# Optimization experiments

Measured on AMD Instinct MI355X. Metric: run time of the kernel, lower is better.

The kernel has to match this reference:

```python
import jax, jax.numpy as jnp
import numpy as np

HEAD, STACK = 8, 2
EPS = 1e-5


def _ln2d(x):
    # F.layer_norm(x, x.size()[1:]): normalize over (seq, feature) jointly, no affine
    m = jnp.mean(x, axis=(1, 2), keepdims=True)
    v = jnp.var(x, axis=(1, 2), keepdims=True)
    return (x - m) / jnp.sqrt(v + EPS)


def setup_inputs() -> dict:
    key = jax.random.key(0)
    ks = jax.random.split(key, 8)
    B, S, V, E, D, C = 64, 1024, 8000, 200, 200, 31
    g = lambda k, shape, sc: (jax.random.normal(k, shape, jnp.float32) * sc)
    return dict(
        x=jax.random.randint(ks[0], (B, S), 0, V),
        embed=g(ks[1], (V, E), 0.02),
        pos=g(ks[2], (S, E), 0.02),
        Wp=g(ks[3], (E, D), 0.05), bp=jnp.zeros((D,), jnp.float32),
        Wm=g(ks[4], (D * HEAD, D), 0.05), bm=jnp.zeros((D,), jnp.float32),
        W1=g(ks[5], (D, D), 0.05), b1=jnp.zeros((D,), jnp.float32),
        W2=g(ks[6], (D, D), 0.05), b2=jnp.zeros((D,), jnp.float32),
        Wd=g(ks[7], (D, C), 0.05), bd=jnp.zeros((C,), jnp.float32),
    )


def reference(x, embed, pos, Wp, bp, Wm, bm, W1, b1, W2, b2, Wd, bd):
    h = embed[x] + pos                       # [B,S,200]
    scale = jnp.sqrt(jnp.asarray(Wp.shape[1], jnp.float32))
    for _ in range(STACK):                   # weights shared across stacks (aliased in torch)
        r = h
        p = h @ Wp + bp                      # q = k = v (same aliased Linear in torch)
        a = jax.nn.softmax(jnp.einsum('bsd,btd->bst', p, p) / scale, axis=-1)
        c = jnp.einsum('bst,btd->bsd', a, p)  # [B,S,200]
        cat = jnp.tile(c, (1, 1, HEAD))       # all heads identical -> concat = tile
        h = _ln2d(cat @ Wm + bm + r)
        r = h
        ff = jax.nn.relu(h @ W1 + b1) @ W2 + b2
        h = _ln2d(ff + r)
    return h[:, -1, :] @ Wd + bd             # [B, class_num]; dropout = identity (eval)
```

## Files before the change

kernel.cpp:

```cpp
#include <hip/hip_runtime.h>
#include <cstddef>
#include <cstdint>
#include <cmath>

#define BDIM  64
#define SDIM  1024
#define DDIM  200
#define DPAD  224
#define PSTRIDE 232
#define CDIM  31
#define NSTACK 2
#define EPS   1e-5f
#define LN_N  204800.0f

typedef __attribute__((ext_vector_type(8))) short short8;
typedef __attribute__((ext_vector_type(4))) short short4_t;
typedef __attribute__((ext_vector_type(4))) float f32x4;

__device__ __forceinline__ short f2bf(float f) {
    union { float f; unsigned u; } v; v.f = f;
    unsigned r = v.u + 0x7FFFu + ((v.u >> 16) & 1u);
    return (short)(r >> 16);
}
__device__ __forceinline__ float bf2f(short s) {
    union { unsigned u; float f; } v; v.u = ((unsigned)(unsigned short)s) << 16;
    return v.f;
}
__device__ __forceinline__ unsigned cvtpk_bf16(float a, float b) {
    unsigned r;
    asm volatile("v_cvt_pk_bf16_f32 %0, %1, %2" : "=v"(r) : "v"(a), "v"(b));
    return r;
}
__device__ __forceinline__ void gload_lds16(const short* g, short* l) {
    __builtin_amdgcn_global_load_lds(
        (const __attribute__((address_space(1))) void*)g,
        (__attribute__((address_space(3))) void*)l, 16, 0, 0);
}

__global__ void prep_kernel(const float* __restrict__ Wp, const float* __restrict__ bp,
                            const float* __restrict__ Wm, const float* __restrict__ bm,
                            const float* __restrict__ W1, const float* __restrict__ b1,
                            const float* __restrict__ W2, const float* __restrict__ b2,
                            short* __restrict__ WtP, short* __restrict__ WtM,
                            short* __restrict__ Wt1, short* __restrict__ Wt2,
                            float* __restrict__ bpP, float* __restrict__ bmP,
                            float* __restrict__ b1P, float* __restrict__ b2P,
                            float* __restrict__ csP, float* __restrict__ cs1)
{
    int idx = blockIdx.x * 256 + threadIdx.x;
    if (idx >= DPAD * DPAD) return;
    int n = idx / DPAD, k = idx - n * DPAD;
    bool valid = (n < DDIM) && (k < DDIM);
    WtP[idx] = valid ? f2bf(Wp[(size_t)k * DDIM + n]) : 0;
    Wt1[idx] = valid ? f2bf(W1[(size_t)k * DDIM + n]) : 0;
    Wt2[idx] = valid ? f2bf(W2[(size_t)k * DDIM + n]) : 0;
    float s = 0.f;
    if (valid) {
        #pragma unroll
        for (int blk = 0; blk < 8; ++blk)
            s += Wm[(size_t)(blk * DDIM + k) * DDIM + n];
    }
    WtM[idx] = valid ? f2bf(s) : 0;
    if (idx < DPAD) {
        bpP[idx] = idx < DDIM ? bp[idx] : 0.f;
        bmP[idx] = idx < DDIM ? bm[idx] : 0.f;
        b1P[idx] = idx < DDIM ? b1[idx] : 0.f;
        b2P[idx] = idx < DDIM ? b2[idx] : 0.f;
        float sp = 0.f, s1 = 0.f;
        if (idx < DDIM) {
            for (int kk = 0; kk < DDIM; ++kk) {
                sp += bf2f(f2bf(Wp[(size_t)kk * DDIM + idx]));
                s1 += bf2f(f2bf(W1[(size_t)kk * DDIM + idx]));
            }
        }
        csP[idx] = sp;
        cs1[idx] = s1;
    }
}

__global__ void embed_kernel(const int* __restrict__ x, const float* __restrict__ embed,
                             const float* __restrict__ pos, short* __restrict__ h)
{
    const int row = blockIdx.x;
    const int n = threadIdx.x;
    if (n >= DPAD) return;
    const int s = row & (SDIM - 1);
    const int tok = x[row];
    float v = (n < DDIM) ? embed[(size_t)tok * DDIM + n] + pos[(size_t)s * DDIM + n] : 0.f;
    h[(size_t)row * DPAD + n] = (n < DDIM) ? f2bf(v) : (short)0;
}

#define WSLICE 7168
#define GBUFSZ 11264
__global__ __launch_bounds__(256, 2)
void gemm_bf(const short* __restrict__ act, const float* __restrict__ actParts,
             const short* __restrict__ Wt, const float* __restrict__ bias,
             const float* __restrict__ csW,
             const short* __restrict__ res, const float* __restrict__ resParts,
             short* __restrict__ out, float* __restrict__ parts,
             int doRelu, int outStride)
{
    __shared__ short SB[2][GBUFSZ];

    const int tid  = threadIdx.x;
    const int wave = tid >> 6, lane = tid & 63;
    const int lo   = lane & 15, hi = lane >> 4;
    const int mblk = blockIdx.x * 128;

    auto stage = [&](int ks, int buf) {
        for (int c = wave; c < 22; c += 4) {
            if (c < 14) {
                int row = c * 16 + (lane >> 2);
                int kc  = (lane & 3) ^ ((row >> 1) & 3);
                gload_lds16(Wt + (size_t)row * DPAD + ks * 32 + kc * 8,
                            &SB[buf][c * 512 + lane * 8]);
            } else {
                int ci  = c - 14;
                int row = ci * 16 + (lane >> 2);
                int kc  = (lane & 3) ^ ((row >> 1) & 3);
                gload_lds16(act + (size_t)(mblk + row) * DPAD + ks * 32 + kc * 8,
                            &SB[buf][WSLICE + ci * 512 + lane * 8]);
            }
        }
    };

    f32x4 acc[2][14];
    #pragma unroll
    for (int mt = 0; mt < 2; ++mt)
        #pragma unroll
        for (int nt = 0; nt < 14; ++nt) acc[mt][nt] = (f32x4){0.f, 0.f, 0.f, 0.f};

    stage(0, 0);
    __syncthreads();

    #pragma unroll
    for (int ks = 0; ks < 7; ++ks) {
        const int cur = ks & 1;
        if (ks < 6) stage(ks + 1, cur ^ 1);

        short8 af[2];
        #pragma unroll
        for (int mt = 0; mt < 2; ++mt) {
            int arow = wave * 32 + mt * 16 + lo;
            af[mt] = *(const short8*)&SB[cur][WSLICE + arow * 32
                                             + ((hi * 8) ^ (((arow >> 1) & 3) << 3))];
        }
        #pragma unroll
        for (int nt = 0; nt < 14; ++nt) {
            int brow = nt * 16 + lo;
            short8 bf_ = *(const short8*)&SB[cur][brow * 32
                                                 + ((hi * 8) ^ (((brow >> 1) & 3) << 3))];
            acc[0][nt] = __builtin_amdgcn_mfma_f32_16x16x32_bf16(af[0], bf_, acc[0][nt], 0, 0, 0);
            acc[1][nt] = __builtin_amdgcn_mfma_f32_16x16x32_bf16(af[1], bf_, acc[1][nt], 0, 0, 0);
        }
        __syncthreads();
    }

    const int bb = mblk >> 10;
    float inv_a = 1.f, corr = 0.f;
    if (actParts) {
        float mean = actParts[bb * 2] / LN_N;
        inv_a = rsqrtf(actParts[bb * 2 + 1] / LN_N - mean * mean + EPS);
        corr = mean * inv_a;
    }
    float mean_r = 0.f, inv_r = 1.f;
    if (resParts) {
        mean_r = resParts[bb * 2] / LN_N;
        inv_r = rsqrtf(resParts[bb * 2 + 1] / LN_N - mean_r * mean_r + EPS);
    }

    float s = 0.f, s2 = 0.f;
    #pragma unroll
    for (int mt = 0; mt < 2; ++mt) {
        #pragma unroll
        for (int nt = 0; nt < 14; ++nt) {
            const int n = nt * 16 + lo;
            const float bn = bias[n];
            const float cw = actParts ? csW[n] : 0.f;
            float v[4];
            #pragma unroll
            for (int r = 0; r < 4; ++r)
                v[r] = acc[mt][nt][r] * inv_a + bn - corr * cw;
            if (res) {
                #pragma unroll
                for (int r = 0; r < 4; ++r) {
                    int m = mblk + wave * 32 + mt * 16 + hi * 4 + r;
                    v[r] += (bf2f(res[(size_t)m * DPAD + n]) - mean_r) * inv_r;
                }
            }
            if (doRelu)
                #pragma unroll
                for (int r = 0; r < 4; ++r) v[r] = fmaxf(v[r], 0.f);
            if (n >= DDIM)
                #pragma unroll
                for (int r = 0; r < 4; ++r) v[r] = 0.f;
            if (parts)
                #pragma unroll
                for (int r = 0; r < 4; ++r) { s += v[r]; s2 = fmaf(v[r], v[r], s2); }
            #pragma unroll
            for (int r = 0; r < 4; ++r) {
                int m = mblk + wave * 32 + mt * 16 + hi * 4 + r;
                out[(size_t)m * outStride + n] = f2bf(v[r]);
            }
        }
    }

    if (parts) {
        __shared__ float rs[4], rq[4];
        #pragma unroll
        for (int off = 32; off; off >>= 1) {
            s  += __shfl_down(s, off);
            s2 += __shfl_down(s2, off);
        }
        if (lane == 0) { rs[wave] = s; rq[wave] = s2; }
        __syncthreads();
        if (tid == 0) {
            atomicAdd(&parts[bb * 2],     rs[0] + rs[1] + rs[2] + rs[3]);
            atomicAdd(&parts[bb * 2 + 1], rq[0] + rq[1] + rq[2] + rq[3]);
        }
    }
}

__global__ void vt_kernel(const short* __restrict__ p, short* __restrict__ pt)
{
    __shared__ short T[32][33];
    const int b  = blockIdx.z;
    const int s0 = blockIdx.x * 32;
    const int d0 = blockIdx.y * 32;
    const int t  = threadIdx.x;
    const int row = t >> 3, c4 = (t & 7) * 4;
    short4_t v = *(const short4_t*)(p + ((size_t)b * SDIM + s0 + row) * PSTRIDE + d0 + c4);
    #pragma unroll
    for (int j = 0; j < 4; ++j) T[row][c4 + j] = v[j];
    __syncthreads();
    short4_t o;
    #pragma unroll
    for (int j = 0; j < 4; ++j) o[j] = T[c4 + j][row];
    *(short4_t*)(pt + ((size_t)b * DPAD + d0 + row) * SDIM + s0 + c4) = o;
}

__global__ __launch_bounds__(256, 2)
void attn_kernel(const short* __restrict__ pbf, const short* __restrict__ pt,
                 short* __restrict__ c, float qscale)
{
    __shared__ short Kbuf[2][7680];
    __shared__ short Vbuf[2][6656];

    const int bid = blockIdx.x;
    const int wg  = (bid & 7) * 64 + (bid >> 3);
    const int b   = wg >> 3;
    const int q0  = (wg & 7) * 128;

    const int tid  = threadIdx.x;
    const int wave = tid >> 6;
    const int lane = tid & 63;
    const int lo   = lane & 15;
    const int hi   = lane >> 4;

    const short* pb  = pbf + (size_t)b * SDIM * PSTRIDE;
    const short* ptb = pt  + (size_t)b * DPAD * SDIM;

    auto stage = [&](int kt2, int bufIdx) {
        const short* ks = pb + (size_t)kt2 * 32 * PSTRIDE + lane * 8;
        #pragma unroll
        for (int i = 0; i < 15; ++i)
            gload_lds16(ks + i * 512, &Kbuf[bufIdx][i * 512]);
        #pragma unroll
        for (int i = 0; i < 13; ++i) {
            int e = i * 512 + lane * 8;
            int d = e >> 5;
            int cc = (e & 31) ^ (((d >> 1) & 3) << 3);
            gload_lds16(ptb + (size_t)d * SDIM + kt2 * 32 + cc, &Vbuf[bufIdx][i * 512]);
        }
    };

    short8 qf[2][7];
    #pragma unroll
    for (int qt = 0; qt < 2; ++qt)
        #pragma unroll
        for (int ks = 0; ks < 7; ++ks) {
            short8 q = *(const short8*)(pb + (size_t)(q0 + wave * 32 + qt * 16 + lo) * PSTRIDE
                                        + ks * 32 + hi * 8);
            short8 qs;
            #pragma unroll
            for (int j = 0; j < 8; ++j) qs[j] = f2bf(bf2f(q[j]) * qscale);
            qf[qt][ks] = qs;
        }

    f32x4 o[2][13];
    float m[2], ell[2];
    #pragma unroll
    for (int qt = 0; qt < 2; ++qt) {
        #pragma unroll
        for (int n = 0; n < 13; ++n) o[qt][n] = (f32x4){0.f, 0.f, 0.f, 0.f};
        m[qt] = -1e30f; ell[qt] = 0.f;
    }

    if (wave == 0) stage(0, 0);
    __syncthreads();

    for (int kt = 0; kt < 32; ++kt) {
        const int cur = kt & 1;
        if (kt < 31 && wave == ((kt + 1) & 3)) stage(kt + 1, cur ^ 1);

        f32x4 sacc[2][2];
        #pragma unroll
        for (int qt = 0; qt < 2; ++qt)
            #pragma unroll
            for (int t = 0; t < 2; ++t) sacc[qt][t] = (f32x4){0.f, 0.f, 0.f, 0.f};
        __builtin_amdgcn_s_setprio(1);
        #pragma unroll
        for (int t = 0; t < 2; ++t)
            #pragma unroll
            for (int ks = 0; ks < 7; ++ks) {
                short8 kf = *(const short8*)(&Kbuf[cur][(t * 16 + lo) * PSTRIDE + ks * 32 + hi * 8]);
                sacc[0][t] = __builtin_amdgcn_mfma_f32_16x16x32_bf16(kf, qf[0][ks], sacc[0][t], 0, 0, 0);
                sacc[1][t] = __builtin_amdgcn_mfma_f32_16x16x32_bf16(kf, qf[1][ks], sacc[1][t], 0, 0, 0);
            }
        __builtin_amdgcn_s_setprio(0);

        short8 pa[2];
        #pragma unroll
        for (int qt = 0; qt < 2; ++qt) {
            float mx = fmaxf(fmaxf(fmaxf(sacc[qt][0][0], sacc[qt][0][1]),
                                   fmaxf(sacc[qt][0][2], sacc[qt][0][3])),
                             fmaxf(fmaxf(sacc[qt][1][0], sacc[qt][1][1]),
                                   fmaxf(sacc[qt][1][2], sacc[qt][1][3])));
            mx = fmaxf(mx, __shfl_xor(mx, 16));
            mx = fmaxf(mx, __shfl_xor(mx, 32));
            if (__any(mx > m[qt] + 11.5f)) {
                float mn = fmaxf(m[qt], mx);
                float al = exp2f(m[qt] - mn);
                m[qt] = mn; ell[qt] *= al;
                float alr[4];
                #pragma unroll
                for (int r = 0; r < 4; ++r) alr[r] = __shfl(al, hi * 4 + r);
                #pragma unroll
                for (int n = 0; n < 13; ++n)
                    #pragma unroll
                    for (int r = 0; r < 4; ++r) o[qt][n][r] *= alr[r];
            }
            float p[2][4]; float rsum = 0.f;
            #pragma unroll
            for (int t = 0; t < 2; ++t)
                #pragma unroll
                for (int r = 0; r < 4; ++r) {
                    p[t][r] = exp2f(sacc[qt][t][r] - m[qt]);
                    rsum += p[t][r];
                }
            rsum += __shfl_xor(rsum, 16);
            rsum += __shfl_xor(rsum, 32);
            ell[qt] += rsum;
            unsigned pk01_0 = cvtpk_bf16(p[0][0], p[0][1]);
            unsigned pk23_0 = cvtpk_bf16(p[0][2], p[0][3]);
            unsigned pk01_1 = cvtpk_bf16(p[1][0], p[1][1]);
            unsigned pk23_1 = cvtpk_bf16(p[1][2], p[1][3]);
            const int srcA = lo + ((hi & 1) * 2) * 16;
            const int srcB = srcA + 16;
            int a0 = __shfl((int)pk01_0, srcA), a1 = __shfl((int)pk01_1, srcA);
            int b0 = __shfl((int)pk23_0, srcA), b1 = __shfl((int)pk23_1, srcA);
            int c0 = __shfl((int)pk01_0, srcB), c1 = __shfl((int)pk01_1, srcB);
            int d0 = __shfl((int)pk23_0, srcB), d1 = __shfl((int)pk23_1, srcB);
            const bool thi = (hi >> 1) != 0;
            union { short8 s; int u[4]; } pu;
            pu.u[0] = thi ? a1 : a0;
            pu.u[1] = thi ? b1 : b0;
            pu.u[2] = thi ? c1 : c0;
            pu.u[3] = thi ? d1 : d0;
            pa[qt] = pu.s;
        }

        __builtin_amdgcn_s_setprio(1);
        #pragma unroll
        for (int n = 0; n < 13; ++n) {
            int d = n * 16 + lo;
            int addr = d * 32 + ((hi * 8) ^ (((d >> 1) & 3) << 3));
            short8 vf = *(const short8*)(&Vbuf[cur][addr]);
            o[0][n] = __builtin_amdgcn_mfma_f32_16x16x32_bf16(pa[0], vf, o[0][n], 0, 0, 0);
            o[1][n] = __builtin_amdgcn_mfma_f32_16x16x32_bf16(pa[1], vf, o[1][n], 0, 0, 0);
        }
        __builtin_amdgcn_s_setprio(0);

        __syncthreads();
    }

    #pragma unroll
    for (int qt = 0; qt < 2; ++qt) {
        float inv_l = 1.f / ell[qt];
        float invr[4];
        #pragma unroll
        for (int r = 0; r < 4; ++r) invr[r] = __shfl(inv_l, hi * 4 + r);
        #pragma unroll
        for (int n = 0; n < 13; ++n) {
            int dcol = n * 16 + lo;
            #pragma unroll
            for (int r = 0; r < 4; ++r) {
                size_t row = (size_t)b * SDIM + q0 + wave * 32 + qt * 16 + hi * 4 + r;
                c[row * DPAD + dcol] = f2bf(o[qt][n][r] * invr[r]);
            }
        }
        #pragma unroll
        for (int r = 0; r < 4; ++r) {
            size_t row = (size_t)b * SDIM + q0 + wave * 32 + qt * 16 + hi * 4 + r;
            c[row * DPAD + 208 + lo] = 0;
        }
    }
}

__global__ void final_kernel(const short* __restrict__ y, const float* __restrict__ parts,
                             const float* __restrict__ Wd, const float* __restrict__ bd,
                             float* __restrict__ out)
{
    const int b = blockIdx.x;
    const float sum = parts[b * 2], sq = parts[b * 2 + 1];
    const float mean = sum / LN_N;
    const float inv  = rsqrtf(sq / LN_N - mean * mean + EPS);
    __shared__ float hrow[DDIM];
    const short* row = y + ((size_t)b * SDIM + SDIM - 1) * DPAD;
    for (int d = threadIdx.x; d < DDIM; d += blockDim.x)
        hrow[d] = (bf2f(row[d]) - mean) * inv;
    __syncthreads();
    if (threadIdx.x < CDIM) {
        float acc = bd[threadIdx.x];
        for (int d = 0; d < DDIM; ++d)
            acc = fmaf(hrow[d], Wd[(size_t)d * CDIM + threadIdx.x], acc);
        out[(size_t)b * CDIM + threadIdx.x] = acc;
    }
}

extern "C" void kernel_launch(void* const* d_in, const int* in_sizes, int n_in,
                              void* d_out, int out_size, void* d_ws, size_t ws_size,
                              hipStream_t stream)
{
    const int*   x     = (const int*)  d_in[0];
    const float* embed = (const float*)d_in[1];
    const float* pos   = (const float*)d_in[2];
    const float* Wp    = (const float*)d_in[3];
    const float* bp    = (const float*)d_in[4];
    const float* Wm    = (const float*)d_in[5];
    const float* bm    = (const float*)d_in[6];
    const float* W1    = (const float*)d_in[7];
    const float* b1    = (const float*)d_in[8];
    const float* W2    = (const float*)d_in[9];
    const float* b2    = (const float*)d_in[10];
    const float* Wd    = (const float*)d_in[11];
    const float* bd    = (const float*)d_in[12];
    float* out = (float*)d_out;

    const size_t HB = (size_t)BDIM * SDIM * DPAD;
    const size_t PB = (size_t)BDIM * SDIM * PSTRIDE;

    short* h_bf  = (short*)d_ws;
    short* p_bf  = h_bf  + HB;
    short* pt    = p_bf  + PB;
    short* cb_bf = pt    + HB;
    short* yA    = cb_bf + HB;
    short* yB    = yA    + HB;
    short* WtP   = yB + HB;
    short* WtM   = WtP + DPAD * DPAD;
    short* Wt1   = WtM + DPAD * DPAD;
    short* Wt2   = Wt1 + DPAD * DPAD;
    float* bpP   = (float*)(Wt2 + DPAD * DPAD);
    float* bmP   = bpP + DPAD;
    float* b1P   = bmP + DPAD;
    float* b2P   = b1P + DPAD;
    float* csP   = b2P + DPAD;
    float* cs1   = csP + DPAD;
    float* parts = cs1 + DPAD;
    const size_t need = (size_t)((char*)(parts + 4 * BDIM * 2) - (char*)d_ws);
    if (ws_size < need) return;

    float* pA1 = parts;
    float* pB1 = parts + BDIM * 2;
    float* pA2 = parts + 2 * BDIM * 2;
    float* pB2 = parts + 3 * BDIM * 2;

    prep_kernel<<<dim3((DPAD * DPAD + 255) / 256), dim3(256), 0, stream>>>(
        Wp, bp, Wm, bm, W1, b1, W2, b2, WtP, WtM, Wt1, Wt2, bpP, bmP, b1P, b2P, csP, cs1);
    embed_kernel<<<dim3(BDIM * SDIM), dim3(256), 0, stream>>>(x, embed, pos, h_bf);
    hipMemsetAsync(parts, 0, 4 * BDIM * 2 * sizeof(float), stream);

    const float qscale = 1.44269504f / sqrtf((float)DDIM);
    const dim3 tgrid(SDIM / 32, DPAD / 32, BDIM);

    gemm_bf<<<dim3(512), dim3(256), 0, stream>>>(h_bf, nullptr, WtP, bpP, nullptr,
                                                 nullptr, nullptr, p_bf, nullptr, 0, PSTRIDE);
    vt_kernel<<<tgrid, dim3(256), 0, stream>>>(p_bf, pt);
    attn_kernel<<<dim3(512), dim3(256), 0, stream>>>(p_bf, pt, cb_bf, qscale);
    gemm_bf<<<dim3(512), dim3(256), 0, stream>>>(cb_bf, nullptr, WtM, bmP, nullptr,
                                                 h_bf, nullptr, yA, pA1, 0, DPAD);
    gemm_bf<<<dim3(512), dim3(256), 0, stream>>>(yA, pA1, Wt1, b1P, cs1,
                                                 nullptr, nullptr, cb_bf, nullptr, 1, DPAD);
    gemm_bf<<<dim3(512), dim3(256), 0, stream>>>(cb_bf, nullptr, Wt2, b2P, nullptr,
                                                 yA, pA1, yB, pB1, 0, DPAD);
    gemm_bf<<<dim3(512), dim3(256), 0, stream>>>(yB, pB1, WtP, bpP, csP,
                                                 nullptr, nullptr, p_bf, nullptr, 0, PSTRIDE);
    vt_kernel<<<tgrid, dim3(256), 0, stream>>>(p_bf, pt);
    attn_kernel<<<dim3(512), dim3(256), 0, stream>>>(p_bf, pt, cb_bf, qscale);
    gemm_bf<<<dim3(512), dim3(256), 0, stream>>>(cb_bf, nullptr, WtM, bmP, nullptr,
                                                 yB, pB1, h_bf, pA2, 0, DPAD);
    gemm_bf<<<dim3(512), dim3(256), 0, stream>>>(h_bf, pA2, Wt1, b1P, cs1,
                                                 nullptr, nullptr, cb_bf, nullptr, 1, DPAD);
    gemm_bf<<<dim3(512), dim3(256), 0, stream>>>(cb_bf, nullptr, Wt2, b2P, nullptr,
                                                 h_bf, pA2, yA, pB2, 0, DPAD);
    final_kernel<<<dim3(BDIM), dim3(64), 0, stream>>>(yA, pB2, Wd, bd, out);
}
```

Baseline: 436.3 us.

## Software-pipeline attention QK/PV, stage GEMM epilogue via LDS, vectorize embed

The attention loop is restructured so the QK^T scores and softmax for tile kt+1 are computed while the PV MFMAs for tile kt run. K and V are staged separately, with K prefetched two tiles ahead, and the rescale of the output accumulator is applied after PV. The GEMM epilogue now writes accumulators to LDS as bf16 and then does row-contiguous vectorized loads and stores of bias, residual and output, replacing scattered 2-byte accesses. The embed kernel becomes a grid-stride loop with float4 loads. Round-tripping accumulators through bf16 before bias and normalization adds rounding error, and the pipelining raises register pressure.

```diff
diff --git a/kernel.cpp b/kernel.cpp
--- a/kernel.cpp
+++ b/kernel.cpp
@@ -81,17 +81,28 @@
 __global__ void embed_kernel(const int* __restrict__ x, const float* __restrict__ embed,
                              const float* __restrict__ pos, short* __restrict__ h)
 {
-    const int row = blockIdx.x;
-    const int n = threadIdx.x;
-    if (n >= DPAD) return;
-    const int s = row & (SDIM - 1);
-    const int tok = x[row];
-    float v = (n < DDIM) ? embed[(size_t)tok * DDIM + n] + pos[(size_t)s * DDIM + n] : 0.f;
-    h[(size_t)row * DPAD + n] = (n < DDIM) ? f2bf(v) : (short)0;
+    const int total = BDIM * SDIM * (DPAD / 4);
+    for (int i = blockIdx.x * 256 + threadIdx.x; i < total; i += gridDim.x * 256) {
+        const int row = i / (DPAD / 4);
+        const int n0  = (i - row * (DPAD / 4)) * 4;
+        short4_t o;
+        if (n0 >= DDIM) {
+            o[0] = o[1] = o[2] = o[3] = 0;
+        } else {
+            const int s = row & (SDIM - 1);
+            const int tok = x[row];
+            const float4 e  = *(const float4*)(embed + (size_t)tok * DDIM + n0);
+            const float4 p4 = *(const float4*)(pos + (size_t)s * DDIM + n0);
+            o[0] = f2bf(e.x + p4.x); o[1] = f2bf(e.y + p4.y);
+            o[2] = f2bf(e.z + p4.z); o[3] = f2bf(e.w + p4.w);
+        }
+        *(short4_t*)(h + (size_t)row * DPAD + n0) = o;
+    }
 }
 
 #define WSLICE 7168
 #define GBUFSZ 11264
+#define SSTRIDE 236
 __global__ __launch_bounds__(256, 2)
 void gemm_bf(const short* __restrict__ act, const float* __restrict__ actParts,
              const short* __restrict__ Wt, const float* __restrict__ bias,
@@ -100,7 +111,7 @@
              short* __restrict__ out, float* __restrict__ parts,
              int doRelu, int outStride)
 {
-    __shared__ short SB[2][GBUFSZ];
+    __shared__ short MEM[128 * SSTRIDE];
 
     const int tid  = threadIdx.x;
     const int wave = tid >> 6, lane = tid & 63;
@@ -108,18 +119,19 @@
     const int mblk = blockIdx.x * 128;
 
     auto stage = [&](int ks, int buf) {
+        short* base = buf ? (MEM + GBUFSZ) : MEM;
         for (int c = wave; c < 22; c += 4) {
             if (c < 14) {
                 int row = c * 16 + (lane >> 2);
                 int kc  = (lane & 3) ^ ((row >> 1) & 3);
                 gload_lds16(Wt + (size_t)row * DPAD + ks * 32 + kc * 8,
-                            &SB[buf][c * 512 + lane * 8]);
+                            base + c * 512 + lane * 8);
             } else {
                 int ci  = c - 14;
                 int row = ci * 16 + (lane >> 2);
                 int kc  = (lane & 3) ^ ((row >> 1) & 3);
                 gload_lds16(act + (size_t)(mblk + row) * DPAD + ks * 32 + kc * 8,
-                            &SB[buf][WSLICE + ci * 512 + lane * 8]);
+                            base + WSLICE + ci * 512 + lane * 8);
             }
         }
     };
@@ -137,24 +149,35 @@
     for (int ks = 0; ks < 7; ++ks) {
         const int cur = ks & 1;
         if (ks < 6) stage(ks + 1, cur ^ 1);
+        const short* B_ = cur ? (MEM + GBUFSZ) : MEM;
 
         short8 af[2];
         #pragma unroll
         for (int mt = 0; mt < 2; ++mt) {
             int arow = wave * 32 + mt * 16 + lo;
-            af[mt] = *(const short8*)&SB[cur][WSLICE + arow * 32
-                                             + ((hi * 8) ^ (((arow >> 1) & 3) << 3))];
+            af[mt] = *(const short8*)&B_[WSLICE + arow * 32
+                                         + ((hi * 8) ^ (((arow >> 1) & 3) << 3))];
         }
         #pragma unroll
         for (int nt = 0; nt < 14; ++nt) {
             int brow = nt * 16 + lo;
-            short8 bf_ = *(const short8*)&SB[cur][brow * 32
-                                                 + ((hi * 8) ^ (((brow >> 1) & 3) << 3))];
+            short8 bf_ = *(const short8*)&B_[brow * 32
+                                             + ((hi * 8) ^ (((brow >> 1) & 3) << 3))];
             acc[0][nt] = __builtin_amdgcn_mfma_f32_16x16x32_bf16(af[0], bf_, acc[0][nt], 0, 0, 0);
             acc[1][nt] = __builtin_amdgcn_mfma_f32_16x16x32_bf16(af[1], bf_, acc[1][nt], 0, 0, 0);
         }
         __syncthreads();
     }
+
+    #pragma unroll
+    for (int mt = 0; mt < 2; ++mt)
+        #pragma unroll
+        for (int nt = 0; nt < 14; ++nt)
+            #pragma unroll
+            for (int r = 0; r < 4; ++r)
+                MEM[(wave * 32 + mt * 16 + hi * 4 + r) * SSTRIDE + nt * 16 + lo]
+                    = f2bf(acc[mt][nt][r]);
+    __syncthreads();
 
     const int bb = mblk >> 10;
     float inv_a = 1.f, corr = 0.f;
@@ -169,40 +192,47 @@
         inv_r = rsqrtf(resParts[bb * 2 + 1] / LN_N - mean_r * mean_r + EPS);
     }
 
+    const int row = tid >> 1;
+    const int octb = (tid & 1) * 14;
+    const size_t gm = (size_t)(mblk + row);
     float s = 0.f, s2 = 0.f;
     #pragma unroll
-    for (int mt = 0; mt < 2; ++mt) {
-        #pragma unroll
-        for (int nt = 0; nt < 14; ++nt) {
-            const int n = nt * 16 + lo;
-            const float bn = bias[n];
-            const float cw = actParts ? csW[n] : 0.f;
-            float v[4];
-            #pragma unroll
-            for (int r = 0; r < 4; ++r)
-                v[r] = acc[mt][nt][r] * inv_a + bn - corr * cw;
-            if (res) {
-                #pragma unroll
-                for (int r = 0; r < 4; ++r) {
-                    int m = mblk + wave * 32 + mt * 16 + hi * 4 + r;
-                    v[r] += (bf2f(res[(size_t)m * DPAD + n]) - mean_r) * inv_r;
-                }
-            }
-            if (doRelu)
-                #pragma unroll
-                for (int r = 0; r < 4; ++r) v[r] = fmaxf(v[r], 0.f);
-            if (n >= DDIM)
-                #pragma unroll
-                for (int r = 0; r < 4; ++r) v[r] = 0.f;
-            if (parts)
-                #pragma unroll
-                for (int r = 0; r < 4; ++r) { s += v[r]; s2 = fmaf(v[r], v[r], s2); }
-            #pragma unroll
-            for (int r = 0; r < 4; ++r) {
-                int m = mblk + wave * 32 + mt * 16 + hi * 4 + r;
-                out[(size_t)m * outStride + n] = f2bf(v[r]);
-            }
-        }
+    for (int o8 = 0; o8 < 14; ++o8) {
+        const int n0 = (octb + o8) * 8;
+        short8 cv = *(const short8*)&MEM[row * SSTRIDE + n0];
+        float4 b4a = *(const float4*)(bias + n0);
+        float4 b4b = *(const float4*)(bias + n0 + 4);
+        float v[8];
+        v[0] = bf2f(cv[0]) * inv_a + b4a.x; v[1] = bf2f(cv[1]) * inv_a + b4a.y;
+        v[2] = bf2f(cv[2]) * inv_a + b4a.z; v[3] = bf2f(cv[3]) * inv_a + b4a.w;
+        v[4] = bf2f(cv[4]) * inv_a + b4b.x; v[5] = bf2f(cv[5]) * inv_a + b4b.y;
+        v[6] = bf2f(cv[6]) * inv_a + b4b.z; v[7] = bf2f(cv[7]) * inv_a + b4b.w;
+        if (actParts) {
+            float4 c4a = *(const float4*)(csW + n0);
+            float4 c4b = *(const float4*)(csW + n0 + 4);
+            v[0] -= corr * c4a.x; v[1] -= corr * c4a.y;
+            v[2] -= corr * c4a.z; v[3] -= corr * c4a.w;
+            v[4] -= corr * c4b.x; v[5] -= corr * c4b.y;
+            v[6] -= corr * c4b.z; v[7] -= corr * c4b.w;
+        }
+        if (res) {
+            short8 rv = *(const short8*)(res + gm * DPAD + n0);
+            #pragma unroll
+            for (int j = 0; j < 8; ++j) v[j] += (bf2f(rv[j]) - mean_r) * inv_r;
+        }
+        if (doRelu)
+            #pragma unroll
+            for (int j = 0; j < 8; ++j) v[j] = fmaxf(v[j], 0.f);
+        #pragma unroll
+        for (int j = 0; j < 8; ++j)
+            if (n0 + j >= DDIM) v[j] = 0.f;
+        if (parts)
+            #pragma unroll
+            for (int j = 0; j < 8; ++j) { s += v[j]; s2 = fmaf(v[j], v[j], s2); }
+        short8 ov;
+        #pragma unroll
+        for (int j = 0; j < 8; ++j) ov[j] = f2bf(v[j]);
+        *(short8*)(out + gm * outStride + n0) = ov;
     }
 
     if (parts) {
@@ -260,17 +290,19 @@
     const short* pb  = pbf + (size_t)b * SDIM * PSTRIDE;
     const short* ptb = pt  + (size_t)b * DPAD * SDIM;
 
-    auto stage = [&](int kt2, int bufIdx) {
+    auto stageK = [&](int kt2, int buf) {
         const short* ks = pb + (size_t)kt2 * 32 * PSTRIDE + lane * 8;
         #pragma unroll
         for (int i = 0; i < 15; ++i)
-            gload_lds16(ks + i * 512, &Kbuf[bufIdx][i * 512]);
+            gload_lds16(ks + i * 512, &Kbuf[buf][i * 512]);
+    };
+    auto stageV = [&](int kt2, int buf) {
         #pragma unroll
         for (int i = 0; i < 13; ++i) {
             int e = i * 512 + lane * 8;
             int d = e >> 5;
             int cc = (e & 31) ^ (((d >> 1) & 3) << 3);
-            gload_lds16(ptb + (size_t)d * SDIM + kt2 * 32 + cc, &Vbuf[bufIdx][i * 512]);
+            gload_lds16(ptb + (size_t)d * SDIM + kt2 * 32 + cc, &Vbuf[buf][i * 512]);
         }
     };
 
@@ -296,30 +328,11 @@
         m[qt] = -1e30f; ell[qt] = 0.f;
     }
 
-    if (wave == 0) stage(0, 0);
-    __syncthreads();
-
-    for (int kt = 0; kt < 32; ++kt) {
-        const int cur = kt & 1;
-        if (kt < 31 && wave == ((kt + 1) & 3)) stage(kt + 1, cur ^ 1);
-
-        f32x4 sacc[2][2];
-        #pragma unroll
-        for (int qt = 0; qt < 2; ++qt)
-            #pragma unroll
-            for (int t = 0; t < 2; ++t) sacc[qt][t] = (f32x4){0.f, 0.f, 0.f, 0.f};
-        __builtin_amdgcn_s_setprio(1);
-        #pragma unroll
-        for (int t = 0; t < 2; ++t)
-            #pragma unroll
-            for (int ks = 0; ks < 7; ++ks) {
-                short8 kf = *(const short8*)(&Kbuf[cur][(t * 16 + lo) * PSTRIDE + ks * 32 + hi * 8]);
-                sacc[0][t] = __builtin_amdgcn_mfma_f32_16x16x32_bf16(kf, qf[0][ks], sacc[0][t], 0, 0, 0);
-                sacc[1][t] = __builtin_amdgcn_mfma_f32_16x16x32_bf16(kf, qf[1][ks], sacc[1][t], 0, 0, 0);
-            }
-        __builtin_amdgcn_s_setprio(0);
-
-        short8 pa[2];
+    f32x4 sacc[2][2];
+    short8 pa_prev[2], pa_next[2];
+    float al_s[2]; bool resc[2];
+
+    auto parta = [&]() {
         #pragma unroll
         for (int qt = 0; qt < 2; ++qt) {
             float mx = fmaxf(fmaxf(fmaxf(sacc[qt][0][0], sacc[qt][0][1]),
@@ -328,18 +341,14 @@
                                    fmaxf(sacc[qt][1][2], sacc[qt][1][3])));
             mx = fmaxf(mx, __shfl_xor(mx, 16));
             mx = fmaxf(mx, __shfl_xor(mx, 32));
-            if (__any(mx > m[qt] + 11.5f)) {
+            float al = 1.f;
+            resc[qt] = __any(mx > m[qt] + 11.5f);
+            if (resc[qt]) {
                 float mn = fmaxf(m[qt], mx);
-                float al = exp2f(m[qt] - mn);
-                m[qt] = mn; ell[qt] *= al;
-                float alr[4];
-                #pragma unroll
-                for (int r = 0; r < 4; ++r) alr[r] = __shfl(al, hi * 4 + r);
-                #pragma unroll
-                for (int n = 0; n < 13; ++n)
-                    #pragma unroll
-                    for (int r = 0; r < 4; ++r) o[qt][n][r] *= alr[r];
+                al = exp2f(m[qt] - mn);
+                m[qt] = mn;
             }
+            al_s[qt] = al;
             float p[2][4]; float rsum = 0.f;
             #pragma unroll
             for (int t = 0; t < 2; ++t)
@@ -350,7 +359,7 @@
                 }
             rsum += __shfl_xor(rsum, 16);
             rsum += __shfl_xor(rsum, 32);
-            ell[qt] += rsum;
+            ell[qt] = ell[qt] * al + rsum;
             unsigned pk01_0 = cvtpk_bf16(p[0][0], p[0][1]);
             unsigned pk23_0 = cvtpk_bf16(p[0][2], p[0][3]);
             unsigned pk01_1 = cvtpk_bf16(p[1][0], p[1][1]);
@@ -367,7 +376,53 @@
             pu.u[1] = thi ? b1 : b0;
             pu.u[2] = thi ? c1 : c0;
             pu.u[3] = thi ? d1 : d0;
-            pa[qt] = pu.s;
+            pa_next[qt] = pu.s;
+        }
+    };
+
+    if (wave == 0) { stageK(0, 0); stageV(0, 0); }
+    if (wave == 1) stageK(1, 1);
+    __syncthreads();
+    {
+        #pragma unroll
+        for (int qt = 0; qt < 2; ++qt)
+            #pragma unroll
+            for (int t = 0; t < 2; ++t) sacc[qt][t] = (f32x4){0.f, 0.f, 0.f, 0.f};
+        #pragma unroll
+        for (int t = 0; t < 2; ++t)
+            #pragma unroll
+            for (int ks = 0; ks < 7; ++ks) {
+                short8 kf = *(const short8*)(&Kbuf[0][(t * 16 + lo) * PSTRIDE + ks * 32 + hi * 8]);
+                sacc[0][t] = __builtin_amdgcn_mfma_f32_16x16x32_bf16(kf, qf[0][ks], sacc[0][t], 0, 0, 0);
+                sacc[1][t] = __builtin_amdgcn_mfma_f32_16x16x32_bf16(kf, qf[1][ks], sacc[1][t], 0, 0, 0);
+            }
+        parta();
+        pa_prev[0] = pa_next[0];
+        pa_prev[1] = pa_next[1];
+    }
+    __syncthreads();
+
+    for (int kt = 0; kt < 32; ++kt) {
+        const int cur = kt & 1;
+        if (kt < 30 && wave == (kt & 3)) stageK(kt + 2, cur);
+        if (kt < 31 && wave == ((kt + 2) & 3)) stageV(kt + 1, cur ^ 1);
+
+        const bool have_next = (kt < 31);
+        if (have_next) {
+            #pragma unroll
+            for (int qt = 0; qt < 2; ++qt)
+                #pragma unroll
+                for (int t = 0; t < 2; ++t) sacc[qt][t] = (f32x4){0.f, 0.f, 0.f, 0.f};
+            __builtin_amdgcn_s_setprio(1);
+            #pragma unroll
+            for (int t = 0; t < 2; ++t)
+                #pragma unroll
+                for (int ks = 0; ks < 7; ++ks) {
+                    short8 kf = *(const short8*)(&Kbuf[cur ^ 1][(t * 16 + lo) * PSTRIDE + ks * 32 + hi * 8]);
+                    sacc[0][t] = __builtin_amdgcn_mfma_f32_16x16x32_bf16(kf, qf[0][ks], sacc[0][t], 0, 0, 0);
+                    sacc[1][t] = __builtin_amdgcn_mfma_f32_16x16x32_bf16(kf, qf[1][ks], sacc[1][t], 0, 0, 0);
+                }
+            __builtin_amdgcn_s_setprio(0);
         }
 
         __builtin_amdgcn_s_setprio(1);
@@ -376,11 +431,28 @@
             int d = n * 16 + lo;
             int addr = d * 32 + ((hi * 8) ^ (((d >> 1) & 3) << 3));
             short8 vf = *(const short8*)(&Vbuf[cur][addr]);
-            o[0][n] = __builtin_amdgcn_mfma_f32_16x16x32_bf16(pa[0], vf, o[0][n], 0, 0, 0);
-            o[1][n] = __builtin_amdgcn_mfma_f32_16x16x32_bf16(pa[1], vf, o[1][n], 0, 0, 0);
+            o[0][n] = __builtin_amdgcn_mfma_f32_16x16x32_bf16(pa_prev[0], vf, o[0][n], 0, 0, 0);
+            o[1][n] = __builtin_amdgcn_mfma_f32_16x16x32_bf16(pa_prev[1], vf, o[1][n], 0, 0, 0);
         }
         __builtin_amdgcn_s_setprio(0);
 
+        if (have_next) {
+            parta();
+            #pragma unroll
+            for (int qt = 0; qt < 2; ++qt) {
+                if (resc[qt]) {
+                    float alr[4];
+                    #pragma unroll
+                    for (int r = 0; r < 4; ++r) alr[r] = __shfl(al_s[qt], hi * 4 + r);
+                    #pragma unroll
+                    for (int n = 0; n < 13; ++n)
+                        #pragma unroll
+                        for (int r = 0; r < 4; ++r) o[qt][n][r] *= alr[r];
+                }
+            }
+            pa_prev[0] = pa_next[0];
+            pa_prev[1] = pa_next[1];
+        }
         __syncthreads();
     }
 
@@ -477,7 +549,7 @@
 
     prep_kernel<<<dim3((DPAD * DPAD + 255) / 256), dim3(256), 0, stream>>>(
         Wp, bp, Wm, bm, W1, b1, W2, b2, WtP, WtM, Wt1, Wt2, bpP, bmP, b1P, b2P, csP, cs1);
-    embed_kernel<<<dim3(BDIM * SDIM), dim3(256), 0, stream>>>(x, embed, pos, h_bf);
+    embed_kernel<<<dim3(2048), dim3(256), 0, stream>>>(x, embed, pos, h_bf);
     hipMemsetAsync(parts, 0, 4 * BDIM * 2 * sizeof(float), stream);
 
     const float qscale = 1.44269504f / sqrtf((float)DDIM);
```

New measurement: 524.1 us. 20.1% more time.
